# Kernel optimization log

Hardware: AMD Instinct MI355X
Metric: run time of the kernel (lower is better)

The kernel has to match this reference:

```python
import jax, jax.numpy as jnp
import numpy as np

B, S, H, NH, DH, L, V, FF = 8, 512, 768, 12, 64, 12, 21128, 3072
PROMPT_LEN = 128
EPS = 1e-12  # BERT LayerNorm eps
NEG = -1e9


def _ln(x, g, b):
    m = jnp.mean(x, axis=-1, keepdims=True)
    xc = x - m
    v = jnp.mean(xc * xc, axis=-1, keepdims=True)
    return xc * jax.lax.rsqrt(v + EPS) * g + b


def setup_inputs() -> dict:
    key = jax.random.key(0)
    ks = jax.random.split(key, 16)
    def p(k, *shape):
        return (jax.random.normal(k, shape, jnp.float32) * 0.02)
    input_ids = jax.random.randint(ks[0], (B, S), 0, V)
    labels = jax.random.randint(ks[1], (B, S), 0, V)
    labels = labels.at[:, :PROMPT_LEN].set(-100)  # prefix = prompt, ignored in CE
    inp = dict(
        input_ids=input_ids,
        labels=labels,
        word_emb=p(ks[2], V, H),
        pos_emb=p(ks[3], S, H),
        type_emb=p(ks[4], 2, H),
        emb_ln_g=jnp.ones((H,), jnp.float32),
        emb_ln_b=jnp.zeros((H,), jnp.float32),
        Wq=p(ks[5], L, H, H), bq=jnp.zeros((L, H), jnp.float32),
        Wk=p(ks[6], L, H, H), bk=jnp.zeros((L, H), jnp.float32),
        Wv=p(ks[7], L, H, H), bv=jnp.zeros((L, H), jnp.float32),
        Wo=p(ks[8], L, H, H), bo=jnp.zeros((L, H), jnp.float32),
        ln1_g=jnp.ones((L, H), jnp.float32), ln1_b=jnp.zeros((L, H), jnp.float32),
        W1=p(ks[9], L, H, FF), bf1=jnp.zeros((L, FF), jnp.float32),
        W2=p(ks[10], L, FF, H), bf2=jnp.zeros((L, H), jnp.float32),
        ln2_g=jnp.ones((L, H), jnp.float32), ln2_b=jnp.zeros((L, H), jnp.float32),
        Wc=p(ks[11], H, V), bc=jnp.zeros((V,), jnp.float32),
    )
    return inp


def _forward(input_ids, labels, word_emb, pos_emb, type_emb, emb_ln_g, emb_ln_b,
             Wq, bq, Wk, bk, Wv, bv, Wo, bo, ln1_g, ln1_b,
             W1, bf1, W2, bf2, ln2_g, ln2_b, Wc, bc):
    # prefix-LM mask: prompt region fully bidirectional-visible, answer region causal
    prompt_len = jnp.sum(labels[0] == -100)
    i = jnp.arange(S)[:, None]
    j = jnp.arange(S)[None, :]
    mask = (j < prompt_len) | ((j >= prompt_len) & (j <= i))  # [S,S]
    bias = jnp.where(mask, 0.0, NEG).astype(jnp.float32)[None, None]  # [1,1,S,S]

    # embeddings (token_type_ids = 0)
    h = word_emb[input_ids] + pos_emb[None, :, :] + type_emb[0][None, None, :]
    h = _ln(h, emb_ln_g, emb_ln_b)
    scale = 1.0 / np.sqrt(DH).astype(np.float32)

    def layer(h, p):
        (wq, bq_, wk, bk_, wv, bv_, wo, bo_, g1, b1_, w1, bff1, w2, bff2, g2, b2_) = p
        q = (h @ wq + bq_).reshape(B, S, NH, DH).transpose(0, 2, 1, 3)
        k = (h @ wk + bk_).reshape(B, S, NH, DH).transpose(0, 2, 1, 3)
        v = (h @ wv + bv_).reshape(B, S, NH, DH).transpose(0, 2, 1, 3)
        scores = jnp.einsum('bhqd,bhkd->bhqk', q, k) * scale + bias
        attn = jax.nn.softmax(scores, axis=-1)
        ctx = jnp.einsum('bhqk,bhkd->bhqd', attn, v)
        ctx = ctx.transpose(0, 2, 1, 3).reshape(B, S, H)
        h = _ln(h + ctx @ wo + bo_, g1, b1_)
        ff = jax.nn.gelu(h @ w1 + bff1, approximate=False) @ w2 + bff2
        h = _ln(h + ff, g2, b2_)
        return h, None

    h, _ = jax.lax.scan(layer, h, (Wq, bq, Wk, bk, Wv, bv, Wo, bo, ln1_g, ln1_b,
                                   W1, bf1, W2, bf2, ln2_g, ln2_b))
    logits = h @ Wc + bc  # [B,S,V]

    # CrossEntropyLoss(ignore_index=-100), mean over valid tokens
    logp = jax.nn.log_softmax(logits, axis=-1)
    valid = labels != -100
    lab = jnp.where(valid, labels, 0)
    nll = -jnp.take_along_axis(logp, lab[..., None], axis=-1)[..., 0]
    loss = jnp.sum(nll * valid) / jnp.sum(valid).astype(jnp.float32)
    return loss


def reference(input_ids, labels, word_emb, pos_emb, type_emb, emb_ln_g, emb_ln_b,
              Wq, bq, Wk, bk, Wv, bv, Wo, bo, ln1_g, ln1_b,
              W1, bf1, W2, bf2, ln2_g, ln2_b, Wc, bc):
    return _forward(input_ids, labels, word_emb, pos_emb, type_emb, emb_ln_g, emb_ln_b,
                    Wq, bq, Wk, bk, Wv, bv, Wo, bo, ln1_g, ln1_b,
                    W1, bf1, W2, bf2, ln2_g, ln2_b, Wc, bc)
```

## Files before the change

### kernel.cpp

```cpp
#include <hip/hip_runtime.h>
#include <hip/hip_bf16.h>
#include <math.h>

#define BB 8
#define SS 512
#define HH 768
#define NHH 12
#define DHH 64
#define LL 12
#define VV 21128
#define VVP 21248
#define FFF 3072
#define TT (BB*SS)
#define PROMPT 128
#define LN_EPS 1e-12f
#define QKVN (3*HH)

typedef __attribute__((ext_vector_type(8))) short short8;
typedef __attribute__((ext_vector_type(4))) short short4v;
typedef __attribute__((ext_vector_type(4))) float floatx4;
typedef __attribute__((ext_vector_type(16))) float floatx16;

__device__ __forceinline__ float gelu_exact(float x) {
    return 0.5f * x * (1.0f + erff(x * 0.70710678118654752f));
}

__device__ __forceinline__ short f2bs(float x) {
    __hip_bfloat16 h = __float2bfloat16(x);
    return *reinterpret_cast<short*>(&h);
}

__device__ __forceinline__ int pack2(float a, float b) {
    const unsigned int lo = (unsigned short)f2bs(a);
    const unsigned int hi = (unsigned short)f2bs(b);
    return (int)(lo | (hi << 16));
}

union I4S8 { int i[4]; short8 s; };

__device__ __forceinline__ void load16_lds(const void* gptr, void* ldsptr) {
    __builtin_amdgcn_global_load_lds(
        (const __attribute__((address_space(1))) unsigned int*)(unsigned long long)(gptr),
        (__attribute__((address_space(3))) unsigned int*)(unsigned long long)(ldsptr),
        16, 0, 0);
}

__global__ __launch_bounds__(256) void gemm_mfma(
    const __hip_bfloat16* __restrict__ A,
    const __hip_bfloat16* __restrict__ Bt,
    const float* __restrict__ bias,
    float* __restrict__ Cf,
    __hip_bfloat16* __restrict__ Ch,
    int M, int N, int K, int act)
{
    __shared__ __hip_bfloat16 As[128 * 64];
    __shared__ __hip_bfloat16 Bs[128 * 64];

    const int tid  = threadIdx.x;
    const int wid  = tid >> 6;
    const int lane = tid & 63;
    const int row0 = blockIdx.y * 128;
    const int col0 = blockIdx.x * 128;

    const int wm = wid >> 1, wn = wid & 1;
    const int lr = lane >> 4, lc = lane & 15;

    const int nz   = gridDim.z;
    const int Kc   = K / nz;
    const int kbeg = blockIdx.z * Kc;
    if (nz > 1) Cf += (size_t)blockIdx.z * M * N;

    floatx4 acc[4][4] = {};

    const int sRow = tid >> 3;
    const int sC   = (tid & 7) ^ (sRow & 7);
    const __hip_bfloat16* aG[4];
    const __hip_bfloat16* bG[4];
    #pragma unroll
    for (int p = 0; p < 4; ++p) {
        aG[p] = A  + (size_t)(row0 + p * 32 + sRow) * K + kbeg + sC * 8;
        bG[p] = Bt + (size_t)(col0 + p * 32 + sRow) * K + kbeg + sC * 8;
    }
    char* aDst = (char*)As + wid * 1024;
    char* bDst = (char*)Bs + wid * 1024;

    for (int k0 = 0; k0 < Kc; k0 += 64) {
        #pragma unroll
        for (int p = 0; p < 4; ++p) {
            load16_lds(aG[p] + k0, aDst + p * 4096);
            load16_lds(bG[p] + k0, bDst + p * 4096);
        }
        __syncthreads();

        #pragma unroll
        for (int ks = 0; ks < 2; ++ks) {
            short8 af[4], bfr[4];
            #pragma unroll
            for (int mt = 0; mt < 4; ++mt) {
                const int row = wm * 64 + mt * 16 + lc;
                af[mt] = *(const short8*)((const char*)As + row * 128 +
                         ((((ks << 2) | lr) ^ (row & 7)) << 4));
            }
            #pragma unroll
            for (int nt = 0; nt < 4; ++nt) {
                const int row = wn * 64 + nt * 16 + lc;
                bfr[nt] = *(const short8*)((const char*)Bs + row * 128 +
                          ((((ks << 2) | lr) ^ (row & 7)) << 4));
            }
            #pragma unroll
            for (int mt = 0; mt < 4; ++mt)
                #pragma unroll
                for (int nt = 0; nt < 4; ++nt)
                    acc[mt][nt] = __builtin_amdgcn_mfma_f32_16x16x32_bf16(
                        af[mt], bfr[nt], acc[mt][nt], 0, 0, 0);
        }
        __syncthreads();
    }

    #pragma unroll
    for (int mt = 0; mt < 4; ++mt) {
        #pragma unroll
        for (int nt = 0; nt < 4; ++nt) {
            const int n = col0 + wn * 64 + nt * 16 + lc;
            if (n < N) {
                #pragma unroll
                for (int r = 0; r < 4; ++r) {
                    const int m = row0 + wm * 64 + mt * 16 + lr * 4 + r;
                    float v = acc[mt][nt][r];
                    if (bias) v += bias[n];
                    if (act)  v = gelu_exact(v);
                    if (Cf) Cf[(size_t)m * N + n] = v;
                    if (Ch) Ch[(size_t)m * N + n] = __float2bfloat16(v);
                }
            }
        }
    }
}

__global__ void transpose_cvt(
    const float* __restrict__ W, __hip_bfloat16* __restrict__ out,
    int K, int N, long long in_lstride, long long out_lstride,
    int row_off, int out_ld)
{
    __shared__ float t[32][33];
    const int n0 = blockIdx.x * 32;
    const int k0 = blockIdx.y * 32;
    const int z  = blockIdx.z;
    const int tx = threadIdx.x, ty = threadIdx.y;

    const float* Wz = W + (size_t)z * in_lstride;
    __hip_bfloat16* Oz = out + (size_t)z * out_lstride;

    #pragma unroll
    for (int r = 0; r < 4; ++r) {
        const int k = k0 + ty + r * 8;
        const int n = n0 + tx;
        if (k < K && n < N) t[ty + r * 8][tx] = Wz[(size_t)k * N + n];
    }
    __syncthreads();
    #pragma unroll
    for (int r = 0; r < 4; ++r) {
        const int n = n0 + ty + r * 8;
        const int k = k0 + tx;
        if (n < N && k < K)
            Oz[(size_t)(row_off + n) * out_ld + k] = __float2bfloat16(t[tx][ty + r * 8]);
    }
}

__global__ void concat_bias(const float* __restrict__ bq, const float* __restrict__ bk,
                            const float* __restrict__ bv, float* __restrict__ bqkv)
{
    const int i = blockIdx.x * 256 + threadIdx.x;
    if (i >= LL * QKVN) return;
    const int l = i / QKVN, j = i % QKVN;
    float v;
    if (j < HH)            v = bq[l * HH + j];
    else if (j < 2 * HH)   v = bk[l * HH + j - HH];
    else                   v = bv[l * HH + j - 2 * HH];
    bqkv[i] = v;
}

__global__ __launch_bounds__(256) void embed_ln(
    const int* __restrict__ ids, const float* __restrict__ we,
    const float* __restrict__ pe, const float* __restrict__ te,
    const float* __restrict__ g, const float* __restrict__ b,
    __hip_bfloat16* __restrict__ h)
{
    const int t = blockIdx.x;
    const int s = t & (SS - 1);
    const int tid = threadIdx.x;
    __shared__ float x[HH];
    __shared__ float red[256];

    const int id = ids[t];
    for (int j = tid; j < HH; j += 256)
        x[j] = we[(size_t)id * HH + j] + pe[(size_t)s * HH + j] + te[j];
    __syncthreads();

    float sum = x[tid] + x[tid + 256] + x[tid + 512];
    red[tid] = sum; __syncthreads();
    for (int s2 = 128; s2 > 0; s2 >>= 1) { if (tid < s2) red[tid] += red[tid + s2]; __syncthreads(); }
    const float mean = red[0] * (1.0f / HH);
    __syncthreads();

    const float c0 = x[tid] - mean, c1 = x[tid + 256] - mean, c2 = x[tid + 512] - mean;
    red[tid] = c0 * c0 + c1 * c1 + c2 * c2; __syncthreads();
    for (int s2 = 128; s2 > 0; s2 >>= 1) { if (tid < s2) red[tid] += red[tid + s2]; __syncthreads(); }
    const float inv = rsqrtf(red[0] * (1.0f / HH) + LN_EPS);

    h[(size_t)t * HH + tid      ] = __float2bfloat16(c0 * inv * g[tid      ] + b[tid      ]);
    h[(size_t)t * HH + tid + 256] = __float2bfloat16(c1 * inv * g[tid + 256] + b[tid + 256]);
    h[(size_t)t * HH + tid + 512] = __float2bfloat16(c2 * inv * g[tid + 512] + b[tid + 512]);
}

__global__ __launch_bounds__(256) void add_ln(
    const __hip_bfloat16* __restrict__ resid, const float* __restrict__ y,
    int P, const float* __restrict__ bias,
    const float* __restrict__ g, const float* __restrict__ b,
    __hip_bfloat16* __restrict__ hout)
{
    const int t = blockIdx.x;
    const int tid = threadIdx.x;
    __shared__ float x[HH];
    __shared__ float red[256];

    for (int j = tid; j < HH; j += 256) {
        float s = __bfloat162float(resid[(size_t)t * HH + j]);
        if (bias) s += bias[j];
        for (int p = 0; p < P; ++p)
            s += y[(size_t)p * TT * HH + (size_t)t * HH + j];
        x[j] = s;
    }
    __syncthreads();

    float sum = x[tid] + x[tid + 256] + x[tid + 512];
    red[tid] = sum; __syncthreads();
    for (int s2 = 128; s2 > 0; s2 >>= 1) { if (tid < s2) red[tid] += red[tid + s2]; __syncthreads(); }
    const float mean = red[0] * (1.0f / HH);
    __syncthreads();

    const float c0 = x[tid] - mean, c1 = x[tid + 256] - mean, c2 = x[tid + 512] - mean;
    red[tid] = c0 * c0 + c1 * c1 + c2 * c2; __syncthreads();
    for (int s2 = 128; s2 > 0; s2 >>= 1) { if (tid < s2) red[tid] += red[tid + s2]; __syncthreads(); }
    const float inv = rsqrtf(red[0] * (1.0f / HH) + LN_EPS);

    hout[(size_t)t * HH + tid      ] = __float2bfloat16(c0 * inv * g[tid      ] + b[tid      ]);
    hout[(size_t)t * HH + tid + 256] = __float2bfloat16(c1 * inv * g[tid + 256] + b[tid + 256]);
    hout[(size_t)t * HH + tid + 512] = __float2bfloat16(c2 * inv * g[tid + 512] + b[tid + 512]);
}

__global__ __launch_bounds__(256) void attn_mfma(
    const float* __restrict__ qkv, __hip_bfloat16* __restrict__ ctx)
{
    const int qb  = blockIdx.x * 128;
    const int hh  = blockIdx.y;
    const int b   = blockIdx.z;
    const int tid = threadIdx.x;
    const int wid = tid >> 6;
    const int lane = tid & 63;
    const int lq = lane & 31;
    const int w  = lane >> 5;

    __shared__ __hip_bfloat16 Kb[64 * 64];
    __shared__ __hip_bfloat16 Vt[64 * 64];

    const int q0 = qb + wid * 32;
    const int i  = q0 + lq;

    short8 qf[4];
    {
        const float* qrow = qkv + (size_t)(b * SS + i) * QKVN + hh * DHH;
        #pragma unroll
        for (int kt = 0; kt < 4; ++kt) {
            const float4 x0 = *(const float4*)(qrow + kt * 16 + w * 8);
            const float4 x1 = *(const float4*)(qrow + kt * 16 + w * 8 + 4);
            short8 q8;
            q8[0] = f2bs(x0.x * 0.125f); q8[1] = f2bs(x0.y * 0.125f);
            q8[2] = f2bs(x0.z * 0.125f); q8[3] = f2bs(x0.w * 0.125f);
            q8[4] = f2bs(x1.x * 0.125f); q8[5] = f2bs(x1.y * 0.125f);
            q8[6] = f2bs(x1.z * 0.125f); q8[7] = f2bs(x1.w * 0.125f);
            qf[kt] = q8;
        }
    }

    floatx16 acc_o[2] = {};
    float m_run = -1e30f, l_run = 0.f;

    const int skey = tid >> 2;
    const int sd4  = (tid & 3) << 2;
    const int vd   = tid & 63;
    const int vk0  = (tid >> 6) << 4;

    const int kmax = (qb + 128 > PROMPT) ? (qb + 128) : PROMPT;

    for (int j0 = 0; j0 < kmax; j0 += 64) {
        {
            const float* kg = qkv + (size_t)(b * SS + j0 + skey) * QKVN + HH + hh * DHH;
            char* krow = (char*)Kb + skey * 128;
            const int sw = (skey & 7) << 4;
            #pragma unroll
            for (int x = 0; x < 4; ++x) {
                const float4 f = *(const float4*)(kg + sd4 + 16 * x);
                short4v kv;
                kv[0] = f2bs(f.x); kv[1] = f2bs(f.y); kv[2] = f2bs(f.z); kv[3] = f2bs(f.w);
                *(short4v*)(krow + (((sd4 << 1) + (x << 5)) ^ sw)) = kv;
            }
        }
        {
            const float* vg = qkv + (size_t)(b * SS + j0 + vk0) * QKVN + 2 * HH + hh * DHH + vd;
            char* vrow = (char*)Vt + vd * 128;
            const int sw = (vd & 7) << 4;
            short8 v8a, v8b;
            #pragma unroll
            for (int x = 0; x < 8; ++x) v8a[x] = f2bs(vg[(size_t)x * QKVN]);
            #pragma unroll
            for (int x = 0; x < 8; ++x) v8b[x] = f2bs(vg[(size_t)(x + 8) * QKVN]);
            *(short8*)(vrow + ((vk0 << 1) ^ sw))        = v8a;
            *(short8*)(vrow + (((vk0 << 1) + 16) ^ sw)) = v8b;
        }
        __syncthreads();

        floatx16 s_acc[2];
        #pragma unroll
        for (int mt = 0; mt < 2; ++mt) {
            const char* krow = (const char*)Kb + (mt * 32 + lq) * 128;
            const int sw = (lq & 7) << 4;
            floatx16 acc = {};
            #pragma unroll
            for (int kt = 0; kt < 4; ++kt) {
                const short8 kf = *(const short8*)(krow + ((kt * 32 + w * 16) ^ sw));
                acc = __builtin_amdgcn_mfma_f32_32x32x16_bf16(kf, qf[kt], acc, 0, 0, 0);
            }
            s_acc[mt] = acc;
        }

        const bool tfull = ((j0 + 63) < PROMPT) || ((j0 + 63) <= q0);
        if (!tfull) {
            #pragma unroll
            for (int mt = 0; mt < 2; ++mt)
                #pragma unroll
                for (int r = 0; r < 16; ++r) {
                    const int key = j0 + mt * 32 + (r & 3) + ((r >> 2) << 3) + (w << 2);
                    if (key >= PROMPT && key > i) s_acc[mt][r] = -1e30f;
                }
        }

        float tmax = -1e30f;
        #pragma unroll
        for (int mt = 0; mt < 2; ++mt)
            #pragma unroll
            for (int r = 0; r < 16; ++r) tmax = fmaxf(tmax, s_acc[mt][r]);
        tmax = fmaxf(tmax, __shfl_xor(tmax, 32, 64));
        const float mnew = fmaxf(m_run, tmax);
        const float corr = __expf(m_run - mnew);
        m_run = mnew;
        float psum = 0.f;
        #pragma unroll
        for (int mt = 0; mt < 2; ++mt)
            #pragma unroll
            for (int r = 0; r < 16; ++r) {
                const float p = __expf(s_acc[mt][r] - mnew);
                s_acc[mt][r] = p;
                psum += p;
            }
        l_run = l_run * corr + psum;
        #pragma unroll
        for (int r = 0; r < 16; ++r) { acc_o[0][r] *= corr; acc_o[1][r] *= corr; }

        short8 pbf[4];
        #pragma unroll
        for (int kt = 0; kt < 4; ++kt) {
            const int mt = kt >> 1;
            const int c0 = ((2 * kt) & 3) << 2;
            const int c1 = ((2 * kt + 1) & 3) << 2;
            const int w0 = pack2(s_acc[mt][c0 + 0], s_acc[mt][c0 + 1]);
            const int w1 = pack2(s_acc[mt][c0 + 2], s_acc[mt][c0 + 3]);
            const int w2 = pack2(s_acc[mt][c1 + 0], s_acc[mt][c1 + 1]);
            const int w3 = pack2(s_acc[mt][c1 + 2], s_acc[mt][c1 + 3]);
            const int t0 = __shfl_xor(w0, 32, 64);
            const int t1 = __shfl_xor(w1, 32, 64);
            const int t2 = __shfl_xor(w2, 32, 64);
            const int t3 = __shfl_xor(w3, 32, 64);
            I4S8 u;
            u.i[0] = w ? t2 : w0;
            u.i[1] = w ? t3 : w1;
            u.i[2] = w ? w2 : t0;
            u.i[3] = w ? w3 : t1;
            pbf[kt] = u.s;
        }

        #pragma unroll
        for (int mtd = 0; mtd < 2; ++mtd) {
            const char* vrow = (const char*)Vt + (mtd * 32 + lq) * 128;
            const int sw = (lq & 7) << 4;
            #pragma unroll
            for (int kt = 0; kt < 4; ++kt) {
                const short8 vf = *(const short8*)(vrow + ((kt * 32 + w * 16) ^ sw));
                acc_o[mtd] = __builtin_amdgcn_mfma_f32_32x32x16_bf16(vf, pbf[kt], acc_o[mtd], 0, 0, 0);
            }
        }
        __syncthreads();
    }

    const float lt  = l_run + __shfl_xor(l_run, 32, 64);
    const float inv = 1.0f / lt;
    __hip_bfloat16* crow = ctx + (size_t)(b * SS + i) * HH + hh * DHH;
    #pragma unroll
    for (int mtd = 0; mtd < 2; ++mtd)
        #pragma unroll
        for (int rq = 0; rq < 4; ++rq) {
            short4v o4;
            #pragma unroll
            for (int e = 0; e < 4; ++e)
                o4[e] = f2bs(acc_o[mtd][rq * 4 + e] * inv);
            *(short4v*)(crow + mtd * 32 + rq * 8 + w * 4) = o4;
        }
}

__global__ __launch_bounds__(256) void ce_kernel(
    const float* __restrict__ logits, const int* __restrict__ labels,
    int bidx, float* __restrict__ acc)
{
    const int r = blockIdx.x;
    const int t = bidx * SS + PROMPT + r;
    const float* row = logits + (size_t)r * VV;
    const int tid = threadIdx.x;
    __shared__ float red[256];

    float mx = -1e30f;
    for (int c = tid; c < VV; c += 256) mx = fmaxf(mx, row[c]);
    red[tid] = mx; __syncthreads();
    for (int s2 = 128; s2 > 0; s2 >>= 1) { if (tid < s2) red[tid] = fmaxf(red[tid], red[tid + s2]); __syncthreads(); }
    mx = red[0];
    __syncthreads();

    float se = 0.f;
    for (int c = tid; c < VV; c += 256) se += __expf(row[c] - mx);
    red[tid] = se; __syncthreads();
    for (int s2 = 128; s2 > 0; s2 >>= 1) { if (tid < s2) red[tid] += red[tid + s2]; __syncthreads(); }

    if (tid == 0) {
        const int lab = labels[t];
        if (lab >= 0) {
            const float nll = -(row[lab] - mx - logf(red[0]));
            atomicAdd(&acc[0], nll);
            atomicAdd(&acc[1], 1.0f);
        }
    }
}

__global__ void finalize_kernel(const float* __restrict__ acc, float* __restrict__ out)
{
    out[0] = (acc[1] > 0.f) ? acc[0] / acc[1] : 0.f;
}

extern "C" void kernel_launch(void* const* d_in, const int* in_sizes, int n_in,
                              void* d_out, int out_size, void* d_ws, size_t ws_size,
                              hipStream_t stream)
{
    const int*   input_ids = (const int*)  d_in[0];
    const int*   labels    = (const int*)  d_in[1];
    const float* word_emb  = (const float*)d_in[2];
    const float* pos_emb   = (const float*)d_in[3];
    const float* type_emb  = (const float*)d_in[4];
    const float* emb_ln_g  = (const float*)d_in[5];
    const float* emb_ln_b  = (const float*)d_in[6];
    const float* Wq = (const float*)d_in[7];   const float* bq = (const float*)d_in[8];
    const float* Wk = (const float*)d_in[9];   const float* bk = (const float*)d_in[10];
    const float* Wv = (const float*)d_in[11];  const float* bv = (const float*)d_in[12];
    const float* Wo = (const float*)d_in[13];  const float* bo = (const float*)d_in[14];
    const float* ln1_g = (const float*)d_in[15]; const float* ln1_b = (const float*)d_in[16];
    const float* W1 = (const float*)d_in[17];  const float* bf1 = (const float*)d_in[18];
    const float* W2 = (const float*)d_in[19];  const float* bf2 = (const float*)d_in[20];
    const float* ln2_g = (const float*)d_in[21]; const float* ln2_b = (const float*)d_in[22];
    const float* Wc = (const float*)d_in[23];  const float* bc = (const float*)d_in[24];

    float* fws = (float*)d_ws;
    float* qkv  = fws;
    float* lg   = qkv;
    float* part = qkv;
    float* tmp  = qkv + (size_t)TT * QKVN;
    float* bqkv = tmp + (size_t)TT * HH;
    float* acc  = bqkv + (size_t)LL * QKVN;

    __hip_bfloat16* bws = (__hip_bfloat16*)(acc + 8);
    __hip_bfloat16* h    = bws;
    __hip_bfloat16* ctx  = h    + (size_t)TT * HH;
    __hip_bfloat16* ff1  = ctx  + (size_t)TT * HH;
    __hip_bfloat16* qkvw = ff1  + (size_t)TT * FFF;
    __hip_bfloat16* wot  = qkvw + (size_t)LL * QKVN * HH;
    __hip_bfloat16* w1t  = wot  + (size_t)LL * HH * HH;
    __hip_bfloat16* w2t  = w1t  + (size_t)LL * FFF * HH;
    __hip_bfloat16* wct  = w2t  + (size_t)LL * HH * FFF;

    hipMemsetAsync(acc, 0, 2 * sizeof(float), stream);

    const dim3 tb(32, 8);
    transpose_cvt<<<dim3(24, 24, LL), tb, 0, stream>>>(Wq, qkvw, HH, HH,
        (long long)HH * HH, (long long)QKVN * HH, 0, HH);
    transpose_cvt<<<dim3(24, 24, LL), tb, 0, stream>>>(Wk, qkvw, HH, HH,
        (long long)HH * HH, (long long)QKVN * HH, HH, HH);
    transpose_cvt<<<dim3(24, 24, LL), tb, 0, stream>>>(Wv, qkvw, HH, HH,
        (long long)HH * HH, (long long)QKVN * HH, 2 * HH, HH);
    transpose_cvt<<<dim3(24, 24, LL), tb, 0, stream>>>(Wo, wot, HH, HH,
        (long long)HH * HH, (long long)HH * HH, 0, HH);
    transpose_cvt<<<dim3(96, 24, LL), tb, 0, stream>>>(W1, w1t, HH, FFF,
        (long long)HH * FFF, (long long)FFF * HH, 0, HH);
    transpose_cvt<<<dim3(24, 96, LL), tb, 0, stream>>>(W2, w2t, FFF, HH,
        (long long)FFF * HH, (long long)HH * FFF, 0, FFF);
    transpose_cvt<<<dim3(661, 24, 1), tb, 0, stream>>>(Wc, wct, HH, VV,
        0, 0, 0, HH);
    concat_bias<<<(LL * QKVN + 255) / 256, 256, 0, stream>>>(bq, bk, bv, bqkv);

    embed_ln<<<TT, 256, 0, stream>>>(input_ids, word_emb, pos_emb, type_emb,
                                     emb_ln_g, emb_ln_b, h);

    const dim3 gQKV(QKVN / 128, TT / 128, 1);
    const dim3 gWo (HH / 128,  TT / 128, 2);
    const dim3 gF  (FFF / 128, TT / 128, 1);
    const dim3 gFF2(HH / 128,  TT / 128, 3);
    const dim3 gAttn(SS / 128, NHH, BB);

    for (int l = 0; l < LL; ++l) {
        gemm_mfma<<<gQKV, 256, 0, stream>>>(h, qkvw + (size_t)l * QKVN * HH,
            bqkv + (size_t)l * QKVN, qkv, nullptr, TT, QKVN, HH, 0);

        attn_mfma<<<gAttn, 256, 0, stream>>>(qkv, ctx);

        gemm_mfma<<<gWo, 256, 0, stream>>>(ctx, wot + (size_t)l * HH * HH,
            nullptr, part, nullptr, TT, HH, HH, 0);
        add_ln<<<TT, 256, 0, stream>>>(h, part, 2, bo + (size_t)l * HH,
            ln1_g + (size_t)l * HH, ln1_b + (size_t)l * HH, h);

        gemm_mfma<<<gF, 256, 0, stream>>>(h, w1t + (size_t)l * FFF * HH,
            bf1 + (size_t)l * FFF, nullptr, ff1, TT, FFF, HH, 1);

        gemm_mfma<<<gFF2, 256, 0, stream>>>(ff1, w2t + (size_t)l * HH * FFF,
            nullptr, part, nullptr, TT, HH, FFF, 0);
        add_ln<<<TT, 256, 0, stream>>>(h, part, 3, bf2 + (size_t)l * HH,
            ln2_g + (size_t)l * HH, ln2_b + (size_t)l * HH, h);
    }

    const int Mchunk = SS - PROMPT;
    const dim3 gV(VVP / 128, Mchunk / 128, 1);
    for (int b = 0; b < BB; ++b) {
        const __hip_bfloat16* Arow = h + (size_t)(b * SS + PROMPT) * HH;
        gemm_mfma<<<gV, 256, 0, stream>>>(Arow, wct, bc, lg, nullptr, Mchunk, VV, HH, 0);
        ce_kernel<<<Mchunk, 256, 0, stream>>>(lg, labels, b, acc);
    }

    finalize_kernel<<<1, 1, 0, stream>>>(acc, (float*)d_out);
}
```

Baseline: 4.422 ms.

## Double-buffer GEMM LDS, store QKV in bf16, and use online softmax in CE

```diff
diff --git a/kernel.cpp b/kernel.cpp
--- a/kernel.cpp
+++ b/kernel.cpp
@@ -53,8 +53,8 @@
     __hip_bfloat16* __restrict__ Ch,
     int M, int N, int K, int act)
 {
-    __shared__ __hip_bfloat16 As[128 * 64];
-    __shared__ __hip_bfloat16 Bs[128 * 64];
+    __shared__ __hip_bfloat16 As[2][128 * 64];
+    __shared__ __hip_bfloat16 Bs[2][128 * 64];
 
     const int tid  = threadIdx.x;
     const int wid  = tid >> 6;
@@ -81,30 +81,43 @@
         aG[p] = A  + (size_t)(row0 + p * 32 + sRow) * K + kbeg + sC * 8;
         bG[p] = Bt + (size_t)(col0 + p * 32 + sRow) * K + kbeg + sC * 8;
     }
-    char* aDst = (char*)As + wid * 1024;
-    char* bDst = (char*)Bs + wid * 1024;
-
-    for (int k0 = 0; k0 < Kc; k0 += 64) {
-        #pragma unroll
-        for (int p = 0; p < 4; ++p) {
-            load16_lds(aG[p] + k0, aDst + p * 4096);
-            load16_lds(bG[p] + k0, bDst + p * 4096);
-        }
-        __syncthreads();
-
+
+    const int nIter = Kc >> 6;
+
+#define STAGE(buf, k0elem) do {                                      \
+        char* aD = (char*)As + (buf) * 16384 + wid * 1024;           \
+        char* bD = (char*)Bs + (buf) * 16384 + wid * 1024;           \
+        _Pragma("unroll")                                            \
+        for (int p = 0; p < 4; ++p) {                                \
+            load16_lds(aG[p] + (k0elem), aD + p * 4096);             \
+            load16_lds(bG[p] + (k0elem), bD + p * 4096);             \
+        }                                                            \
+    } while (0)
+
+    STAGE(0, 0);
+    __syncthreads();
+
+    int cur = 0;
+    for (int t = 0; t < nIter; ++t) {
+        if (t + 1 < nIter) STAGE(cur ^ 1, (t + 1) << 6);
+
+        const char* Ab = (const char*)As + cur * 16384;
+        const char* Bb = (const char*)Bs + cur * 16384;
+
+        __builtin_amdgcn_s_setprio(1);
         #pragma unroll
         for (int ks = 0; ks < 2; ++ks) {
             short8 af[4], bfr[4];
             #pragma unroll
             for (int mt = 0; mt < 4; ++mt) {
                 const int row = wm * 64 + mt * 16 + lc;
-                af[mt] = *(const short8*)((const char*)As + row * 128 +
+                af[mt] = *(const short8*)(Ab + row * 128 +
                          ((((ks << 2) | lr) ^ (row & 7)) << 4));
             }
             #pragma unroll
             for (int nt = 0; nt < 4; ++nt) {
                 const int row = wn * 64 + nt * 16 + lc;
-                bfr[nt] = *(const short8*)((const char*)Bs + row * 128 +
+                bfr[nt] = *(const short8*)(Bb + row * 128 +
                           ((((ks << 2) | lr) ^ (row & 7)) << 4));
             }
             #pragma unroll
@@ -114,8 +127,12 @@
                     acc[mt][nt] = __builtin_amdgcn_mfma_f32_16x16x32_bf16(
                         af[mt], bfr[nt], acc[mt][nt], 0, 0, 0);
         }
+        __builtin_amdgcn_s_setprio(0);
+
         __syncthreads();
-    }
+        cur ^= 1;
+    }
+#undef STAGE
 
     #pragma unroll
     for (int mt = 0; mt < 4; ++mt) {
@@ -250,7 +267,7 @@
 }
 
 __global__ __launch_bounds__(256) void attn_mfma(
-    const float* __restrict__ qkv, __hip_bfloat16* __restrict__ ctx)
+    const __hip_bfloat16* __restrict__ qkv, __hip_bfloat16* __restrict__ ctx)
 {
     const int qb  = blockIdx.x * 128;
     const int hh  = blockIdx.y;
@@ -269,52 +286,40 @@
 
     short8 qf[4];
     {
-        const float* qrow = qkv + (size_t)(b * SS + i) * QKVN + hh * DHH;
-        #pragma unroll
-        for (int kt = 0; kt < 4; ++kt) {
-            const float4 x0 = *(const float4*)(qrow + kt * 16 + w * 8);
-            const float4 x1 = *(const float4*)(qrow + kt * 16 + w * 8 + 4);
-            short8 q8;
-            q8[0] = f2bs(x0.x * 0.125f); q8[1] = f2bs(x0.y * 0.125f);
-            q8[2] = f2bs(x0.z * 0.125f); q8[3] = f2bs(x0.w * 0.125f);
-            q8[4] = f2bs(x1.x * 0.125f); q8[5] = f2bs(x1.y * 0.125f);
-            q8[6] = f2bs(x1.z * 0.125f); q8[7] = f2bs(x1.w * 0.125f);
-            qf[kt] = q8;
-        }
+        const __hip_bfloat16* qrow = qkv + (size_t)(b * SS + i) * QKVN + hh * DHH;
+        #pragma unroll
+        for (int kt = 0; kt < 4; ++kt)
+            qf[kt] = *(const short8*)(qrow + kt * 16 + w * 8);
     }
 
     floatx16 acc_o[2] = {};
     float m_run = -1e30f, l_run = 0.f;
 
-    const int skey = tid >> 2;
-    const int sd4  = (tid & 3) << 2;
+    const int kRow = tid >> 3;
+    const int kC   = tid & 7;
     const int vd   = tid & 63;
     const int vk0  = (tid >> 6) << 4;
 
     const int kmax = (qb + 128 > PROMPT) ? (qb + 128) : PROMPT;
 
     for (int j0 = 0; j0 < kmax; j0 += 64) {
+        #pragma unroll
+        for (int x = 0; x < 2; ++x) {
+            const int row = x * 32 + kRow;
+            const __hip_bfloat16* src = qkv + (size_t)(b * SS + j0 + row) * QKVN
+                                        + HH + hh * DHH + ((kC ^ (row & 7)) << 3);
+            load16_lds(src, (char*)Kb + x * 4096 + wid * 1024 + (lane << 4));
+        }
         {
-            const float* kg = qkv + (size_t)(b * SS + j0 + skey) * QKVN + HH + hh * DHH;
-            char* krow = (char*)Kb + skey * 128;
-            const int sw = (skey & 7) << 4;
-            #pragma unroll
-            for (int x = 0; x < 4; ++x) {
-                const float4 f = *(const float4*)(kg + sd4 + 16 * x);
-                short4v kv;
-                kv[0] = f2bs(f.x); kv[1] = f2bs(f.y); kv[2] = f2bs(f.z); kv[3] = f2bs(f.w);
-                *(short4v*)(krow + (((sd4 << 1) + (x << 5)) ^ sw)) = kv;
-            }
-        }
-        {
-            const float* vg = qkv + (size_t)(b * SS + j0 + vk0) * QKVN + 2 * HH + hh * DHH + vd;
+            const short* vg = (const short*)(qkv + (size_t)(b * SS + j0 + vk0) * QKVN
+                                             + 2 * HH + hh * DHH + vd);
             char* vrow = (char*)Vt + vd * 128;
             const int sw = (vd & 7) << 4;
             short8 v8a, v8b;
             #pragma unroll
-            for (int x = 0; x < 8; ++x) v8a[x] = f2bs(vg[(size_t)x * QKVN]);
-            #pragma unroll
-            for (int x = 0; x < 8; ++x) v8b[x] = f2bs(vg[(size_t)(x + 8) * QKVN]);
+            for (int x = 0; x < 8; ++x) v8a[x] = vg[(size_t)x * QKVN];
+            #pragma unroll
+            for (int x = 0; x < 8; ++x) v8b[x] = vg[(size_t)(x + 8) * QKVN];
             *(short8*)(vrow + ((vk0 << 1) ^ sw))        = v8a;
             *(short8*)(vrow + (((vk0 << 1) + 16) ^ sw)) = v8b;
         }
@@ -333,6 +338,10 @@
             }
             s_acc[mt] = acc;
         }
+        #pragma unroll
+        for (int mt = 0; mt < 2; ++mt)
+            #pragma unroll
+            for (int r = 0; r < 16; ++r) s_acc[mt][r] *= 0.125f;
 
         const bool tfull = ((j0 + 63) < PROMPT) || ((j0 + 63) <= q0);
         if (!tfull) {
@@ -425,24 +434,31 @@
     const int t = bidx * SS + PROMPT + r;
     const float* row = logits + (size_t)r * VV;
     const int tid = threadIdx.x;
-    __shared__ float red[256];
-
-    float mx = -1e30f;
-    for (int c = tid; c < VV; c += 256) mx = fmaxf(mx, row[c]);
-    red[tid] = mx; __syncthreads();
-    for (int s2 = 128; s2 > 0; s2 >>= 1) { if (tid < s2) red[tid] = fmaxf(red[tid], red[tid + s2]); __syncthreads(); }
-    mx = red[0];
-    __syncthreads();
-
-    float se = 0.f;
-    for (int c = tid; c < VV; c += 256) se += __expf(row[c] - mx);
-    red[tid] = se; __syncthreads();
-    for (int s2 = 128; s2 > 0; s2 >>= 1) { if (tid < s2) red[tid] += red[tid + s2]; __syncthreads(); }
+    __shared__ float redm[256];
+    __shared__ float reds[256];
+
+    float mx = -1e30f, se = 0.f;
+    for (int c4 = tid; c4 < VV / 4; c4 += 256) {
+        const float4 v = ((const float4*)row)[c4];
+        const float lm = fmaxf(fmaxf(v.x, v.y), fmaxf(v.z, v.w));
+        if (lm > mx) { se *= __expf(mx - lm); mx = lm; }
+        se += __expf(v.x - mx) + __expf(v.y - mx) + __expf(v.z - mx) + __expf(v.w - mx);
+    }
+    redm[tid] = mx; reds[tid] = se; __syncthreads();
+    for (int s2 = 128; s2 > 0; s2 >>= 1) {
+        if (tid < s2) {
+            const float m2 = redm[tid + s2], sv = reds[tid + s2];
+            const float mN = fmaxf(redm[tid], m2);
+            reds[tid] = reds[tid] * __expf(redm[tid] - mN) + sv * __expf(m2 - mN);
+            redm[tid] = mN;
+        }
+        __syncthreads();
+    }
 
     if (tid == 0) {
         const int lab = labels[t];
         if (lab >= 0) {
-            const float nll = -(row[lab] - mx - logf(red[0]));
+            const float nll = -(row[lab] - redm[0] - logf(reds[0]));
             atomicAdd(&acc[0], nll);
             atomicAdd(&acc[1], 1.0f);
         }
@@ -475,18 +491,17 @@
     const float* ln2_g = (const float*)d_in[21]; const float* ln2_b = (const float*)d_in[22];
     const float* Wc = (const float*)d_in[23];  const float* bc = (const float*)d_in[24];
 
-    float* fws = (float*)d_ws;
-    float* qkv  = fws;
-    float* lg   = qkv;
-    float* part = qkv;
-    float* tmp  = qkv + (size_t)TT * QKVN;
-    float* bqkv = tmp + (size_t)TT * HH;
+    float* fws  = (float*)d_ws;
+    float* part = fws;
+    float* lg   = fws;
+    float* bqkv = fws + (size_t)TT * QKVN + (size_t)TT * HH;
     float* acc  = bqkv + (size_t)LL * QKVN;
 
     __hip_bfloat16* bws = (__hip_bfloat16*)(acc + 8);
     __hip_bfloat16* h    = bws;
     __hip_bfloat16* ctx  = h    + (size_t)TT * HH;
     __hip_bfloat16* ff1  = ctx  + (size_t)TT * HH;
+    __hip_bfloat16* qkvb = ff1;
     __hip_bfloat16* qkvw = ff1  + (size_t)TT * FFF;
     __hip_bfloat16* wot  = qkvw + (size_t)LL * QKVN * HH;
     __hip_bfloat16* w1t  = wot  + (size_t)LL * HH * HH;
@@ -523,9 +538,9 @@
 
     for (int l = 0; l < LL; ++l) {
         gemm_mfma<<<gQKV, 256, 0, stream>>>(h, qkvw + (size_t)l * QKVN * HH,
-            bqkv + (size_t)l * QKVN, qkv, nullptr, TT, QKVN, HH, 0);
-
-        attn_mfma<<<gAttn, 256, 0, stream>>>(qkv, ctx);
+            bqkv + (size_t)l * QKVN, nullptr, qkvb, TT, QKVN, HH, 0);
+
+        attn_mfma<<<gAttn, 256, 0, stream>>>(qkvb, ctx);
 
         gemm_mfma<<<gWo, 256, 0, stream>>>(ctx, wot + (size_t)l * HH * HH,
             nullptr, part, nullptr, TT, HH, HH, 0);
```

Measured after the change: 3.923 ms. 11.3% less time.
